# Kernel optimization log

Measured on AMD Instinct MI355X. Metric: run time of the kernel, lower is better.

## Reference

```python
import jax, jax.numpy as jnp
import numpy as np

D_MODEL = 1024
N_HEADS = 16
D_KV = D_MODEL // N_HEADS
MAX_SEQ = 2048
THETA = 10000.0
BATCH = 2
SEQ = 2048


def setup_inputs() -> dict:
    key = jax.random.key(0)
    ks = jax.random.split(key, 5)
    std = np.sqrt(2.0 / (D_MODEL + D_MODEL))
    x = jax.random.normal(ks[0], (BATCH, SEQ, D_MODEL), dtype=jnp.float32)
    wq = jax.random.normal(ks[1], (D_MODEL, D_MODEL), dtype=jnp.float32) * std
    wk = jax.random.normal(ks[2], (D_MODEL, D_MODEL), dtype=jnp.float32) * std
    wv = jax.random.normal(ks[3], (D_MODEL, D_MODEL), dtype=jnp.float32) * std
    wo = jax.random.normal(ks[4], (D_MODEL, D_MODEL), dtype=jnp.float32) * std
    token_positions = jnp.arange(SEQ, dtype=jnp.int32)
    return {"x": x, "wq": wq, "wk": wk, "wv": wv, "wo": wo,
            "token_positions": token_positions}


def _rope_tables():
    freq_range = jnp.arange(D_KV // 2, dtype=jnp.float32)
    freq = 1.0 / (THETA ** (2.0 * freq_range / D_KV))
    pos = jnp.arange(MAX_SEQ, dtype=jnp.float32)
    angs = pos[:, None] * freq[None, :]  # [max_seq, d_kv/2]
    return jnp.cos(angs), jnp.sin(angs)


def _apply_rope(xh, token_positions, cos_t, sin_t):
    # xh: [b, h, s, d_kv]
    cos_f = jnp.repeat(cos_t[token_positions], 2, axis=-1)  # [s, d_kv]
    sin_f = jnp.repeat(sin_t[token_positions], 2, axis=-1)
    pairs = xh.reshape(*xh.shape[:-1], D_KV // 2, 2)
    even, odd = pairs[..., 0], pairs[..., 1]
    rot = jnp.stack([-odd, even], axis=-1).reshape(xh.shape)
    return xh * cos_f + rot * sin_f


def reference(x, wq, wk, wv, wo, token_positions):
    b, s, _ = x.shape
    def heads(y):
        return y.reshape(b, s, N_HEADS, D_KV).transpose(0, 2, 1, 3)  # [b,h,s,d]
    q = heads(jnp.einsum('bsi,oi->bso', x, wq))
    k = heads(jnp.einsum('bsi,oi->bso', x, wk))
    v = heads(jnp.einsum('bsi,oi->bso', x, wv))
    cos_t, sin_t = _rope_tables()
    q = _apply_rope(q, token_positions, cos_t, sin_t)
    k = _apply_rope(k, token_positions, cos_t, sin_t)
    scale = 1.0 / jnp.sqrt(jnp.asarray(D_KV, x.dtype))
    scores = jnp.einsum('bhqd,bhkd->bhqk', q, k) * scale
    causal = jnp.tril(jnp.ones((s, s), dtype=bool))
    scores = jnp.where(causal, scores, -jnp.inf)
    probs = jax.nn.softmax(scores, axis=-1)
    attn = jnp.einsum('bhqk,bhkd->bhqd', probs, v)
    attn = attn.transpose(0, 2, 1, 3).reshape(b, s, D_MODEL)
    return jnp.einsum('bsi,oi->bso', attn, wo)
```

## Files before the change

kernel.cpp:

```cpp
#include <hip/hip_runtime.h>
#include <hip/hip_bf16.h>
#include <math.h>

#define SEQ 2048
#define DM 1024
#define NH 16
#define DKV 64
#define MTOT 4096
#define PST2 72

typedef __attribute__((ext_vector_type(8))) short bf16x8;
typedef __attribute__((ext_vector_type(4))) short s16x4;
typedef __attribute__((ext_vector_type(4))) float f32x4;
typedef unsigned short ushort_t;

__device__ __forceinline__ short f2bf(float f) {
    union { float f; unsigned u; } v; v.f = f;
    unsigned r = v.u + 0x7fffu + ((v.u >> 16) & 1u);
    return (short)(r >> 16);
}

__device__ __forceinline__ bf16x8 cvt8(f32x4 a, f32x4 b) {
    union { __hip_bfloat162 h[4]; bf16x8 v; } u;
    u.h[0] = __float22bfloat162_rn(float2{a[0], a[1]});
    u.h[1] = __float22bfloat162_rn(float2{a[2], a[3]});
    u.h[2] = __float22bfloat162_rn(float2{b[0], b[1]});
    u.h[3] = __float22bfloat162_rn(float2{b[2], b[3]});
    return u.v;
}

__device__ __forceinline__ s16x4 cvt4(float a, float b, float c, float d) {
    union { __hip_bfloat162 h[2]; s16x4 v; } u;
    u.h[0] = __float22bfloat162_rn(float2{a, b});
    u.h[1] = __float22bfloat162_rn(float2{c, d});
    return u.v;
}

__device__ __forceinline__ void gload_lds16(const void* g, void* l) {
    __builtin_amdgcn_global_load_lds(
        (const __attribute__((address_space(1))) unsigned int*)g,
        (__attribute__((address_space(3))) unsigned int*)l, 16, 0, 0);
}

__global__ void prep_kernel(const float* __restrict__ x,
                            const float* __restrict__ wq, const float* __restrict__ wk,
                            const float* __restrict__ wv, const float* __restrict__ wo,
                            ushort_t* __restrict__ Wqkv, ushort_t* __restrict__ xb,
                            ushort_t* __restrict__ Wob,
                            float* __restrict__ cos_t, float* __restrict__ sin_t) {
    const int b = blockIdx.x;
    if (b < 256) {
        int tid = b * 256 + threadIdx.x;
        int i = tid & 31, pos = tid >> 5;
        float freq = expf(-9.210340372f * (float)(2 * i) / 64.0f);
        float ang = (float)pos * freq;
        cos_t[tid] = cosf(ang);
        sin_t[tid] = sinf(ang);
    } else if (b < 768) {
        int tid = (b - 256) * 256 + threadIdx.x;
        int off = tid * 8;
        f32x4 a = ((const f32x4*)(wo + off))[0];
        f32x4 c = ((const f32x4*)(wo + off))[1];
        *(bf16x8*)&Wob[off] = cvt8(a, c);
    } else if (b < 2304) {
        int tid = (b - 768) * 256 + threadIdx.x;
        int z = tid >> 17;
        int off = (tid & 131071) * 8;
        const float* src = (z == 0) ? wq : (z == 1) ? wk : wv;
        f32x4 a = ((const f32x4*)(src + off))[0];
        f32x4 c = ((const f32x4*)(src + off))[1];
        *(bf16x8*)&Wqkv[(size_t)z * 1048576 + off] = cvt8(a, c);
    } else {
        int tid = (b - 2304) * 256 + threadIdx.x;
        int off = tid * 8;
        f32x4 a = ((const f32x4*)(x + off))[0];
        f32x4 c = ((const f32x4*)(x + off))[1];
        *(bf16x8*)&xb[off] = cvt8(a, c);
    }
}

__global__ __launch_bounds__(512) void proj_qkv_kernel(
    const ushort_t* __restrict__ xb, const ushort_t* __restrict__ Wqkv,
    const float* __restrict__ cos_t, const float* __restrict__ sin_t,
    const int* __restrict__ tokpos,
    ushort_t* __restrict__ Qg, ushort_t* __restrict__ Kg, ushort_t* __restrict__ Vt)
{
    __shared__ __align__(16) short lA[2][256 * 64];
    __shared__ __align__(16) short lB[2][256 * 64];

    const int t = threadIdx.x;
    const int lane = t & 63;
    const int wid = t >> 6;
    const int quad = lane >> 4, l16 = lane & 15;
    const int wm = wid >> 2, wn = wid & 3;
    const int Mb = blockIdx.y * 256;
    const int NbG = blockIdx.x * 256;
    const int z = NbG >> 10;
    const int Nb = NbG & 1023;

    f32x4 acc[8][4] = {};

    auto stage = [&](int kt, int buf) {
        const int k0 = kt * 64;
        #pragma unroll
        for (int j = 0; j < 4; ++j) {
            int rbase = wid * 32 + j * 8;
            int row = rbase + (lane >> 3);
            int gch = (lane & 7) ^ (row & 7);
            gload_lds16(xb + (size_t)(Mb + row) * DM + k0 + gch * 8, &lA[buf][rbase * 64]);
        }
        #pragma unroll
        for (int j = 0; j < 4; ++j) {
            int rbase = wid * 32 + j * 8;
            int row = rbase + (lane >> 3);
            int gch = (lane & 7) ^ (row & 7);
            gload_lds16(Wqkv + (size_t)(NbG + row) * DM + k0 + gch * 8, &lB[buf][rbase * 64]);
        }
    };

    stage(0, 0);

    for (int kt = 0; kt < 16; ++kt) {
        const int cur = kt & 1;
        asm volatile("s_waitcnt vmcnt(0)" ::: "memory");
        __builtin_amdgcn_s_barrier();
        if (kt < 15) stage(kt + 1, cur ^ 1);

        #pragma unroll
        for (int ks = 0; ks < 2; ++ks) {
            bf16x8 a[8], b[4];
            #pragma unroll
            for (int mf = 0; mf < 8; ++mf) {
                int row = wm * 128 + mf * 16 + l16;
                int slot = (ks * 4 + quad) ^ (row & 7);
                a[mf] = *(const bf16x8*)&lA[cur][row * 64 + slot * 8];
            }
            #pragma unroll
            for (int nf = 0; nf < 4; ++nf) {
                int row = wn * 64 + nf * 16 + l16;
                int slot = (ks * 4 + quad) ^ (row & 7);
                b[nf] = *(const bf16x8*)&lB[cur][row * 64 + slot * 8];
            }
            __builtin_amdgcn_s_setprio(1);
            #pragma unroll
            for (int mf = 0; mf < 8; ++mf)
                #pragma unroll
                for (int nf = 0; nf < 4; ++nf)
                    acc[mf][nf] = __builtin_amdgcn_mfma_f32_16x16x32_bf16(a[mf], b[nf], acc[mf][nf], 0, 0, 0);
            __builtin_amdgcn_s_setprio(0);
        }
    }

    const int bb = Mb >> 11;
    if (z == 2) {
        #pragma unroll
        for (int mf = 0; mf < 8; ++mf) {
            const int s0 = (Mb + wm * 128 + mf * 16 + quad * 4) & (SEQ - 1);
            #pragma unroll
            for (int nf = 0; nf < 4; ++nf) {
                int col = Nb + wn * 64 + nf * 16 + l16;
                int h = col >> 6, d = col & 63;
                s16x4 pk;
                #pragma unroll
                for (int r = 0; r < 4; ++r) pk[r] = f2bf(acc[mf][nf][r]);
                *(s16x4*)&Vt[((size_t)(bb * NH + h) * DKV + d) * SEQ + s0] = pk;
            }
        }
    } else {
        ushort_t* dst = (z == 0) ? Qg : Kg;
        const float qscale = (z == 0) ? 0.125f : 1.0f;
        #pragma unroll
        for (int mf = 0; mf < 8; ++mf) {
            #pragma unroll
            for (int nf = 0; nf < 4; ++nf) {
                #pragma unroll
                for (int r = 0; r < 4; ++r) {
                    int row = Mb + wm * 128 + mf * 16 + quad * 4 + r;
                    int s = row & (SEQ - 1);
                    int col = Nb + wn * 64 + nf * 16 + l16;
                    int h = col >> 6, d = col & 63;
                    float val = acc[mf][nf][r];
                    float part = __shfl_xor(val, 1, 64);
                    int pos = tokpos[s];
                    int i = d >> 1;
                    float c = cos_t[pos * 32 + i];
                    float sn = sin_t[pos * 32 + i];
                    val = (d & 1) ? (val * c + part * sn) : (val * c - part * sn);
                    val *= qscale;
                    dst[((size_t)(bb * NH + h) * SEQ + s) * DKV + d] = (ushort_t)f2bf(val);
                }
            }
        }
    }
}

__global__ __launch_bounds__(256, 2) void attn_kernel(
    const ushort_t* __restrict__ Q, const ushort_t* __restrict__ K,
    const ushort_t* __restrict__ Vt, ushort_t* __restrict__ O)
{
    __shared__ __align__(16) short lK[2][2][64 * 64];
    __shared__ __align__(16) short lV[2][2][64 * 64];
    __shared__ __align__(16) short lP[4][16 * PST2];

    const int t = threadIdx.x;
    const int lane = t & 63;
    const int wid = t >> 6;
    const int quad = lane >> 4, l16 = lane & 15;
    const int bh = blockIdx.y;
    const int bb = bh >> 4, h = bh & 15;

    const ushort_t* Qb = Q + (size_t)bh * SEQ * DKV;
    const ushort_t* Kb = K + (size_t)bh * SEQ * DKV;
    const ushort_t* Vtb = Vt + (size_t)bh * DKV * SEQ;
    short* myP = lP[wid];

    auto stage = [&](int kb, int buf) {
        #pragma unroll
        for (int hf = 0; hf < 2; ++hf) {
            #pragma unroll
            for (int j = 0; j < 2; ++j) {
                int rbase = wid * 16 + j * 8;
                int row = rbase + (lane >> 3);
                int gch = (lane & 7) ^ (row & 7);
                gload_lds16(Kb + (size_t)(kb + hf * 64 + row) * DKV + gch * 8,
                            &lK[buf][hf][rbase * 64]);
            }
            #pragma unroll
            for (int j = 0; j < 2; ++j) {
                int rbase = wid * 16 + j * 8;
                int row = rbase + (lane >> 3);
                int gch = (lane & 7) ^ (row & 7);
                gload_lds16(Vtb + (size_t)row * SEQ + kb + hf * 64 + gch * 8,
                            &lV[buf][hf][rbase * 64]);
            }
        }
    };

    #pragma unroll 1
    for (int ph = 0; ph < 2; ++ph) {
        const int qt = ph ? (31 - (int)blockIdx.x) : (int)blockIdx.x;
        const int q0w = qt * 64 + wid * 16;
        const int nkt2 = (qt >> 1) + 1;

        bf16x8 bq[2];
        #pragma unroll
        for (int hq = 0; hq < 2; ++hq)
            bq[hq] = *(const bf16x8*)(Qb + (size_t)(q0w + l16) * DKV + hq * 32 + quad * 8);

        f32x4 acc[4] = {};
        float ps = 0.f;

        if (ph) __syncthreads();
        stage(0, 0);

        for (int kt2 = 0; kt2 < nkt2; ++kt2) {
            const int kb128 = kt2 * 128;
            __syncthreads();
            if (kt2 + 1 < nkt2) stage(kb128 + 128, (kt2 + 1) & 1);

            #pragma unroll
            for (int hf = 0; hf < 2; ++hf) {
                const int kbase = kb128 + hf * 64;
                if (kbase > q0w + 15) continue;

                const short* bK = lK[kt2 & 1][hf];
                const short* bV = lV[kt2 & 1][hf];

                bf16x8 ak[4][2];
                #pragma unroll
                for (int mt = 0; mt < 4; ++mt)
                    #pragma unroll
                    for (int hh = 0; hh < 2; ++hh) {
                        int row = mt * 16 + l16;
                        int slot = (hh * 4 + quad) ^ (row & 7);
                        ak[mt][hh] = *(const bf16x8*)&bK[row * 64 + slot * 8];
                    }

                f32x4 st[4];
                __builtin_amdgcn_s_setprio(1);
                #pragma unroll
                for (int mt = 0; mt < 4; ++mt) {
                    f32x4 zz = {};
                    zz = __builtin_amdgcn_mfma_f32_16x16x32_bf16(ak[mt][0], bq[0], zz, 0, 0, 0);
                    zz = __builtin_amdgcn_mfma_f32_16x16x32_bf16(ak[mt][1], bq[1], zz, 0, 0, 0);
                    st[mt] = zz;
                }
                __builtin_amdgcn_s_setprio(0);

                if (kbase + 63 > q0w) {
                    #pragma unroll
                    for (int mt = 0; mt < 4; ++mt) {
                        float pv[4];
                        #pragma unroll
                        for (int r = 0; r < 4; ++r) {
                            int k_abs = kbase + mt * 16 + quad * 4 + r;
                            int q_abs = q0w + l16;
                            pv[r] = (k_abs > q_abs) ? 0.f : __expf(st[mt][r]);
                            ps += pv[r];
                        }
                        *(s16x4*)&myP[l16 * PST2 + mt * 16 + quad * 4] = cvt4(pv[0], pv[1], pv[2], pv[3]);
                    }
                } else {
                    #pragma unroll
                    for (int mt = 0; mt < 4; ++mt) {
                        float pv[4];
                        #pragma unroll
                        for (int r = 0; r < 4; ++r) {
                            pv[r] = __expf(st[mt][r]);
                            ps += pv[r];
                        }
                        *(s16x4*)&myP[l16 * PST2 + mt * 16 + quad * 4] = cvt4(pv[0], pv[1], pv[2], pv[3]);
                    }
                }

                bf16x8 ap[2];
                ap[0] = *(const bf16x8*)&myP[l16 * PST2 + quad * 8];
                ap[1] = *(const bf16x8*)&myP[l16 * PST2 + 32 + quad * 8];

                __builtin_amdgcn_s_setprio(1);
                #pragma unroll
                for (int d = 0; d < 4; ++d) {
                    int row = d * 16 + l16;
                    int slot0 = quad ^ (row & 7);
                    int slot1 = (4 + quad) ^ (row & 7);
                    bf16x8 bv0 = *(const bf16x8*)&bV[row * 64 + slot0 * 8];
                    bf16x8 bv1 = *(const bf16x8*)&bV[row * 64 + slot1 * 8];
                    acc[d] = __builtin_amdgcn_mfma_f32_16x16x32_bf16(ap[0], bv0, acc[d], 0, 0, 0);
                    acc[d] = __builtin_amdgcn_mfma_f32_16x16x32_bf16(ap[1], bv1, acc[d], 0, 0, 0);
                }
                __builtin_amdgcn_s_setprio(0);
            }
        }

        ps += __shfl_xor(ps, 16, 64);
        ps += __shfl_xor(ps, 32, 64);
        float* lLw = (float*)myP;
        if (quad == 0) lLw[l16] = ps;
        f32x4 lv = *(const f32x4*)&lLw[quad * 4];
        f32x4 inv;
        #pragma unroll
        for (int r = 0; r < 4; ++r) inv[r] = 1.0f / lv[r];
        #pragma unroll
        for (int d = 0; d < 4; ++d)
            #pragma unroll
            for (int r = 0; r < 4; ++r) {
                int qrow = q0w + quad * 4 + r;
                int dd = d * 16 + l16;
                O[(size_t)(bb * SEQ + qrow) * DM + h * DKV + dd] = (ushort_t)f2bf(acc[d][r] * inv[r]);
            }
    }
}

__global__ __launch_bounds__(256) void oproj_kernel(
    const ushort_t* __restrict__ A, const ushort_t* __restrict__ B, float* __restrict__ out)
{
    __shared__ __align__(16) short lA[3][128 * 32];
    __shared__ __align__(16) short lB[3][64 * 32];

    const int t = threadIdx.x;
    const int lane = t & 63;
    const int wid = t >> 6;
    const int quad = lane >> 4, l16 = lane & 15;
    const int mh = wid >> 1, nh = wid & 1;
    const int Mb = blockIdx.y * 128;
    const int Nb = blockIdx.x * 64;

    f32x4 acc[4][2] = {};

    auto stage = [&](int buf, int k0) {
        #pragma unroll
        for (int i = 0; i < 2; ++i) {
            int rbase = wid * 32 + i * 16;
            int row = rbase + (lane >> 2);
            int gch = (lane & 3) ^ ((lane >> 3) & 3);
            gload_lds16(A + (size_t)(Mb + row) * DM + k0 + gch * 8, &lA[buf][rbase * 32]);
        }
        {
            int rbase = wid * 16;
            int row = rbase + (lane >> 2);
            int gch = (lane & 3) ^ ((lane >> 3) & 3);
            gload_lds16(B + (size_t)(Nb + row) * DM + k0 + gch * 8, &lB[buf][rbase * 32]);
        }
    };

    stage(0, 0);
    stage(1, 32);

    for (int kt = 0; kt < 32; ++kt) {
        const int cur = kt % 3;
        if (kt == 31) asm volatile("s_waitcnt vmcnt(0)" ::: "memory");
        else          asm volatile("s_waitcnt vmcnt(3)" ::: "memory");
        __builtin_amdgcn_s_barrier();
        if (kt < 30) stage((kt + 2) % 3, kt * 32 + 64);

        bf16x8 a[4], b[2];
        #pragma unroll
        for (int mt = 0; mt < 4; ++mt) {
            int row = mh * 64 + mt * 16 + l16;
            int slot = quad ^ ((l16 >> 1) & 3);
            a[mt] = *(const bf16x8*)&lA[cur][row * 32 + slot * 8];
        }
        #pragma unroll
        for (int nt = 0; nt < 2; ++nt) {
            int row = nh * 32 + nt * 16 + l16;
            int slot = quad ^ ((l16 >> 1) & 3);
            b[nt] = *(const bf16x8*)&lB[cur][row * 32 + slot * 8];
        }
        __builtin_amdgcn_s_setprio(1);
        #pragma unroll
        for (int mt = 0; mt < 4; ++mt)
            #pragma unroll
            for (int nt = 0; nt < 2; ++nt)
                acc[mt][nt] = __builtin_amdgcn_mfma_f32_16x16x32_bf16(a[mt], b[nt], acc[mt][nt], 0, 0, 0);
        __builtin_amdgcn_s_setprio(0);
    }

    #pragma unroll
    for (int mt = 0; mt < 4; ++mt)
        #pragma unroll
        for (int nt = 0; nt < 2; ++nt)
            #pragma unroll
            for (int r = 0; r < 4; ++r) {
                int row = Mb + mh * 64 + mt * 16 + quad * 4 + r;
                int col = Nb + nh * 32 + nt * 16 + l16;
                out[(size_t)row * DM + col] = acc[mt][nt][r];
            }
}

extern "C" void kernel_launch(void* const* d_in, const int* in_sizes, int n_in,
                              void* d_out, int out_size, void* d_ws, size_t ws_size,
                              hipStream_t stream) {
    const float* x  = (const float*)d_in[0];
    const float* wq = (const float*)d_in[1];
    const float* wk = (const float*)d_in[2];
    const float* wv = (const float*)d_in[3];
    const float* wo = (const float*)d_in[4];
    const int* tokpos = (const int*)d_in[5];
    float* out = (float*)d_out;

    char* ws = (char*)d_ws;
    float* cos_t    = (float*)ws;
    float* sin_t    = (float*)(ws + 256 * 1024);
    ushort_t* Wqkv  = (ushort_t*)(ws + 512 * 1024);
    ushort_t* AO    = (ushort_t*)ws;
    ushort_t* Qg    = (ushort_t*)(ws + (size_t)8  * 1024 * 1024);
    ushort_t* Kg    = (ushort_t*)(ws + (size_t)16 * 1024 * 1024);
    ushort_t* Wob   = (ushort_t*)(ws + (size_t)24 * 1024 * 1024);
    ushort_t* xb    = (ushort_t*)d_out;
    ushort_t* Vt    = (ushort_t*)((char*)d_out + (size_t)8 * 1024 * 1024);

    prep_kernel<<<4352, 256, 0, stream>>>(x, wq, wk, wv, wo, Wqkv, xb, Wob, cos_t, sin_t);
    proj_qkv_kernel<<<dim3(3 * DM / 256, MTOT / 256), 512, 0, stream>>>(
        xb, Wqkv, cos_t, sin_t, tokpos, Qg, Kg, Vt);
    attn_kernel<<<dim3(SEQ / 128, 32), 256, 0, stream>>>(Qg, Kg, Vt, AO);
    oproj_kernel<<<dim3(DM / 64, MTOT / 128), 256, 0, stream>>>(AO, Wob, out);
}
```

Baseline: 193.2 us.

## Triple-buffer QKV projection GEMM with BK=32 and deeper prefetch

The QKV projection GEMM moves from a double-buffered K-tile of 64 to a triple-buffered K-tile of 32, prefetching two stages ahead. It waits with vmcnt(4) instead of draining all loads, so global-to-LDS copies overlap more with MFMA work. The LDS swizzle is adapted to 32-wide rows. LDS use drops, but there are twice as many barriers per K loop and less MFMA work between them.

```diff
diff --git a/kernel.cpp b/kernel.cpp
--- a/kernel.cpp
+++ b/kernel.cpp
@@ -85,8 +85,8 @@
     const int* __restrict__ tokpos,
     ushort_t* __restrict__ Qg, ushort_t* __restrict__ Kg, ushort_t* __restrict__ Vt)
 {
-    __shared__ __align__(16) short lA[2][256 * 64];
-    __shared__ __align__(16) short lB[2][256 * 64];
+    __shared__ __align__(16) short lA[3][256 * 32];
+    __shared__ __align__(16) short lB[3][256 * 32];
 
     const int t = threadIdx.x;
     const int lane = t & 63;
@@ -100,55 +100,53 @@
 
     f32x4 acc[8][4] = {};
 
-    auto stage = [&](int kt, int buf) {
-        const int k0 = kt * 64;
-        #pragma unroll
-        for (int j = 0; j < 4; ++j) {
-            int rbase = wid * 32 + j * 8;
-            int row = rbase + (lane >> 3);
-            int gch = (lane & 7) ^ (row & 7);
-            gload_lds16(xb + (size_t)(Mb + row) * DM + k0 + gch * 8, &lA[buf][rbase * 64]);
-        }
-        #pragma unroll
-        for (int j = 0; j < 4; ++j) {
-            int rbase = wid * 32 + j * 8;
-            int row = rbase + (lane >> 3);
-            int gch = (lane & 7) ^ (row & 7);
-            gload_lds16(Wqkv + (size_t)(NbG + row) * DM + k0 + gch * 8, &lB[buf][rbase * 64]);
+    auto stage = [&](int buf, int k0) {
+        #pragma unroll
+        for (int i = 0; i < 2; ++i) {
+            int rbase = wid * 32 + i * 16;
+            int row = rbase + (lane >> 2);
+            int gch = (lane & 3) ^ ((lane >> 3) & 3);
+            gload_lds16(xb + (size_t)(Mb + row) * DM + k0 + gch * 8, &lA[buf][rbase * 32]);
+        }
+        #pragma unroll
+        for (int i = 0; i < 2; ++i) {
+            int rbase = wid * 32 + i * 16;
+            int row = rbase + (lane >> 2);
+            int gch = (lane & 3) ^ ((lane >> 3) & 3);
+            gload_lds16(Wqkv + (size_t)(NbG + row) * DM + k0 + gch * 8, &lB[buf][rbase * 32]);
         }
     };
 
     stage(0, 0);
-
-    for (int kt = 0; kt < 16; ++kt) {
-        const int cur = kt & 1;
-        asm volatile("s_waitcnt vmcnt(0)" ::: "memory");
+    stage(1, 32);
+
+    for (int kt = 0; kt < 32; ++kt) {
+        const int cur = kt % 3;
+        if (kt == 31) asm volatile("s_waitcnt vmcnt(0)" ::: "memory");
+        else          asm volatile("s_waitcnt vmcnt(4)" ::: "memory");
         __builtin_amdgcn_s_barrier();
-        if (kt < 15) stage(kt + 1, cur ^ 1);
-
-        #pragma unroll
-        for (int ks = 0; ks < 2; ++ks) {
-            bf16x8 a[8], b[4];
-            #pragma unroll
-            for (int mf = 0; mf < 8; ++mf) {
-                int row = wm * 128 + mf * 16 + l16;
-                int slot = (ks * 4 + quad) ^ (row & 7);
-                a[mf] = *(const bf16x8*)&lA[cur][row * 64 + slot * 8];
-            }
-            #pragma unroll
-            for (int nf = 0; nf < 4; ++nf) {
-                int row = wn * 64 + nf * 16 + l16;
-                int slot = (ks * 4 + quad) ^ (row & 7);
-                b[nf] = *(const bf16x8*)&lB[cur][row * 64 + slot * 8];
-            }
-            __builtin_amdgcn_s_setprio(1);
-            #pragma unroll
-            for (int mf = 0; mf < 8; ++mf)
-                #pragma unroll
-                for (int nf = 0; nf < 4; ++nf)
-                    acc[mf][nf] = __builtin_amdgcn_mfma_f32_16x16x32_bf16(a[mf], b[nf], acc[mf][nf], 0, 0, 0);
-            __builtin_amdgcn_s_setprio(0);
-        }
+        if (kt < 30) stage((kt + 2) % 3, kt * 32 + 64);
+
+        bf16x8 a[8], b[4];
+        #pragma unroll
+        for (int mf = 0; mf < 8; ++mf) {
+            int row = wm * 128 + mf * 16 + l16;
+            int slot = quad ^ ((l16 >> 1) & 3);
+            a[mf] = *(const bf16x8*)&lA[cur][row * 32 + slot * 8];
+        }
+        #pragma unroll
+        for (int nf = 0; nf < 4; ++nf) {
+            int row = wn * 64 + nf * 16 + l16;
+            int slot = quad ^ ((l16 >> 1) & 3);
+            b[nf] = *(const bf16x8*)&lB[cur][row * 32 + slot * 8];
+        }
+        __builtin_amdgcn_s_setprio(1);
+        #pragma unroll
+        for (int mf = 0; mf < 8; ++mf)
+            #pragma unroll
+            for (int nf = 0; nf < 4; ++nf)
+                acc[mf][nf] = __builtin_amdgcn_mfma_f32_16x16x32_bf16(a[mf], b[nf], acc[mf][nf], 0, 0, 0);
+        __builtin_amdgcn_s_setprio(0);
     }
 
     const int bb = Mb >> 11;
```

Measured after the change: 198.1 us. 1.03x slower.
